# Performance work log

Measured on AMD Instinct MI355X. Metric: run time of the kernel, lower is better.

Reference implementation:

```python
import jax, jax.numpy as jnp
import numpy as np

DIM = 384
HEADS = 6
K = 3  # kernel_size, stride = 1


def setup_inputs() -> dict:
    key = jax.random.key(0)
    ks = jax.random.split(key, 7)
    B, H, W, C = 16, 56, 56, DIM
    sc = 1.0 / np.sqrt(C)
    return {
        "x_map": jax.random.normal(ks[0], (B, H, W, C), dtype=jnp.float32),
        # Linear weights stored [in, out] (torch stores [out, in]; math identical)
        "W_attn": jax.random.normal(ks[1], (C, HEADS * K * K), dtype=jnp.float32) * sc,
        "b_attn": jax.random.normal(ks[2], (HEADS * K * K,), dtype=jnp.float32) * 0.02,
        "W_v": jax.random.normal(ks[3], (C, C), dtype=jnp.float32) * sc,
        "b_v": jax.random.normal(ks[4], (C,), dtype=jnp.float32) * 0.02,
        "W_proj": jax.random.normal(ks[5], (C, C), dtype=jnp.float32) * sc,
        "b_proj": jax.random.normal(ks[6], (C,), dtype=jnp.float32) * 0.02,
    }


def reference(x_map, W_attn, b_attn, W_v, b_v, W_proj, b_proj):
    B, H, W, C = x_map.shape
    k, heads = K, HEADS
    hd = C // heads
    pad = k // 2

    # attention logits per output pixel: [B, H*W, heads, k*k], softmax over window
    a = x_map @ W_attn + b_attn                     # [B,H,W,heads*k*k]
    a = jax.nn.softmax(a.reshape(B, H * W, heads, k * k), axis=-1)

    v = x_map @ W_v + b_v                           # [B,H,W,C]
    vp = jnp.pad(v, ((0, 0), (pad, pad), (pad, pad), (0, 0)))
    # k*k shifted views == F.unfold with row-major (ki,kj) kernel order
    patches = jnp.stack(
        [vp[:, i:i + H, j:j + W, :] for i in range(k) for j in range(k)],
        axis=3,
    )                                               # [B,H,W,k*k,C]
    patches = patches.reshape(B, H * W, k * k, heads, hd)

    # softmax-weighted sum over the k*k window, per head
    y = jnp.einsum('bpKhd,bphK->bphd', patches, a)  # [B,H*W,heads,hd]
    y = y.reshape(B, H, W, C)
    return y @ W_proj + b_proj
```

## Files before the change

### kernel.cpp

```cpp
#include <hip/hip_runtime.h>
#include <math.h>

#define NPIX 50176
#define CDIM 384
#define HEADS 6
#define NLOGIT 54
#define HH 56
#define WW 56

typedef __attribute__((ext_vector_type(8))) __bf16 bf16x8;
typedef __attribute__((ext_vector_type(4))) float f32x4;

__device__ __forceinline__ void glds16(const void* g, void* l) {
  __builtin_amdgcn_global_load_lds(
      (const __attribute__((address_space(1))) unsigned int*)g,
      (__attribute__((address_space(3))) unsigned int*)l, 16, 0, 0);
}

__global__ __launch_bounds__(256) void prep_kernel(
    const float* __restrict__ W_v, const float* __restrict__ W_proj,
    const float* __restrict__ W_attn, const float* __restrict__ b_attn,
    __bf16* __restrict__ Wtv, __bf16* __restrict__ Wtp,
    __bf16* __restrict__ Wta, float* __restrict__ bpad) {
  const int idx = blockIdx.x * 256 + threadIdx.x;
  const int WSZ = CDIM * CDIM;
  if (idx < WSZ) {
    const int n = idx / CDIM, k = idx % CDIM;
    Wtv[idx] = (__bf16)W_v[k * CDIM + n];
    Wtp[idx] = (__bf16)W_proj[k * CDIM + n];
  } else if (idx < WSZ + 64 * CDIM) {
    const int r = idx - WSZ;
    const int n = r / CDIM, k = r % CDIM;
    Wta[r] = (__bf16)((n < NLOGIT) ? W_attn[k * NLOGIT + n] : 0.f);
  } else if (idx < WSZ + 64 * CDIM + 64) {
    const int n = idx - WSZ - 64 * CDIM;
    bpad[n] = (n < NLOGIT) ? b_attn[n] : 0.f;
  }
}

__global__ __launch_bounds__(256) void gemm_v_logit_kernel(
    const float* __restrict__ X, const __bf16* __restrict__ Wtv,
    const float* __restrict__ b_v, __bf16* __restrict__ v,
    const __bf16* __restrict__ Wta, const float* __restrict__ bpad,
    float* __restrict__ attn) {
  __shared__ char smem[34816];
  __bf16 (*As)[32] = (__bf16(*)[32])smem;
  __bf16 (*Bs)[32] = (__bf16(*)[32])(smem + 8192);
  float (*Ls)[68]  = (float(*)[68])smem;

  const int tid  = threadIdx.x;
  const int wave = tid >> 6;
  const int lane = tid & 63;
  const int bm   = blockIdx.x * 128;
  const int lrow  = lane >> 2;
  const int lkoff = (lane & 3) * 8;
  const int frow  = lane & 15;
  const int fk    = (lane >> 4) * 8;

  const bool is_logit = (blockIdx.y == 3);
  const int bn = is_logit ? 0 : blockIdx.y * 128;
  const int wr = (wave >> 1) * 64;
  const int wc = (wave & 1) * 64;

  f32x4 acc[4][4] = {};

  for (int k0 = 0; k0 < CDIM; k0 += 32) {
    const float* gx = X + (size_t)(bm + wave * 32 + lrow) * CDIM + k0 + lkoff;
    const float4 f0 = *(const float4*)(gx + 0);
    const float4 f1 = *(const float4*)(gx + 4);
    const float4 f2 = *(const float4*)(gx + 16 * CDIM + 0);
    const float4 f3 = *(const float4*)(gx + 16 * CDIM + 4);

    if (is_logit) {
      const __bf16* gb = Wta + (size_t)(wave * 16 + lrow) * CDIM + k0 + lkoff;
      glds16(gb, &Bs[wave * 16][0]);
    } else {
      const __bf16* gb = Wtv + (size_t)(bn + wave * 32 + lrow) * CDIM + k0 + lkoff;
      glds16(gb,                     &Bs[wave * 32][0]);
      glds16(gb + 16 * (size_t)CDIM, &Bs[wave * 32 + 16][0]);
    }

    bf16x8 h0, h1;
    h0[0] = (__bf16)f0.x; h0[1] = (__bf16)f0.y; h0[2] = (__bf16)f0.z; h0[3] = (__bf16)f0.w;
    h0[4] = (__bf16)f1.x; h0[5] = (__bf16)f1.y; h0[6] = (__bf16)f1.z; h0[7] = (__bf16)f1.w;
    h1[0] = (__bf16)f2.x; h1[1] = (__bf16)f2.y; h1[2] = (__bf16)f2.z; h1[3] = (__bf16)f2.w;
    h1[4] = (__bf16)f3.x; h1[5] = (__bf16)f3.y; h1[6] = (__bf16)f3.z; h1[7] = (__bf16)f3.w;
    *(bf16x8*)&As[wave * 32 + lrow][lkoff]      = h0;
    *(bf16x8*)&As[wave * 32 + 16 + lrow][lkoff] = h1;
    __syncthreads();

    if (is_logit) {
      bf16x8 a[2], b[4];
      #pragma unroll
      for (int mi = 0; mi < 2; ++mi)
        a[mi] = *(const bf16x8*)&As[wave * 32 + mi * 16 + frow][fk];
      #pragma unroll
      for (int ni = 0; ni < 4; ++ni)
        b[ni] = *(const bf16x8*)&Bs[ni * 16 + frow][fk];
      #pragma unroll
      for (int mi = 0; mi < 2; ++mi)
        #pragma unroll
        for (int ni = 0; ni < 4; ++ni)
          acc[mi][ni] = __builtin_amdgcn_mfma_f32_16x16x32_bf16(
              a[mi], b[ni], acc[mi][ni], 0, 0, 0);
    } else {
      bf16x8 a[4], b[4];
      #pragma unroll
      for (int mi = 0; mi < 4; ++mi)
        a[mi] = *(const bf16x8*)&As[wr + mi * 16 + frow][fk];
      #pragma unroll
      for (int ni = 0; ni < 4; ++ni)
        b[ni] = *(const bf16x8*)&Bs[wc + ni * 16 + frow][fk];
      #pragma unroll
      for (int mi = 0; mi < 4; ++mi)
        #pragma unroll
        for (int ni = 0; ni < 4; ++ni)
          acc[mi][ni] = __builtin_amdgcn_mfma_f32_16x16x32_bf16(
              a[mi], b[ni], acc[mi][ni], 0, 0, 0);
    }
    __syncthreads();
  }

  if (!is_logit) {
    const int orow = (lane >> 4) * 4;
    #pragma unroll
    for (int mi = 0; mi < 4; ++mi) {
      #pragma unroll
      for (int ni = 0; ni < 4; ++ni) {
        const int n = bn + wc + ni * 16 + frow;
        const float bvl = b_v[n];
        #pragma unroll
        for (int r = 0; r < 4; ++r) {
          const int m = bm + wr + mi * 16 + orow + r;
          v[(size_t)m * CDIM + n] = (__bf16)(acc[mi][ni][r] + bvl);
        }
      }
    }
  } else {
    float bvl[4];
    #pragma unroll
    for (int ni = 0; ni < 4; ++ni) bvl[ni] = bpad[ni * 16 + frow];
    const int orow = (lane >> 4) * 4;
    #pragma unroll
    for (int mi = 0; mi < 2; ++mi)
      #pragma unroll
      for (int ni = 0; ni < 4; ++ni)
        #pragma unroll
        for (int r = 0; r < 4; ++r)
          Ls[wave * 32 + mi * 16 + orow + r][ni * 16 + frow] =
              acc[mi][ni][r] + bvl[ni];
    __syncthreads();

    #pragma unroll
    for (int it = 0; it < 3; ++it) {
      const int task = it * 256 + tid;
      const int pl = task / HEADS;
      const int h  = task % HEADS;
      const float* row = &Ls[pl][h * 9];
      float m = row[0];
      #pragma unroll
      for (int w = 1; w < 9; ++w) m = fmaxf(m, row[w]);
      float e[9], s = 0.f;
      #pragma unroll
      for (int w = 0; w < 9; ++w) { e[w] = __expf(row[w] - m); s += e[w]; }
      const float inv = 1.f / s;
      float* op = &attn[(size_t)(bm + pl) * NLOGIT + h * 9];
      #pragma unroll
      for (int w = 0; w < 9; ++w) op[w] = e[w] * inv;
    }
  }
}

__global__ __launch_bounds__(256) void gemm_proj_kernel(
    const __bf16* __restrict__ A, const __bf16* __restrict__ Bt,
    const float* __restrict__ bias, float* __restrict__ Out) {
  __shared__ __bf16 As[128][32];
  __shared__ __bf16 Bs[128][32];

  const int tid  = threadIdx.x;
  const int wave = tid >> 6;
  const int lane = tid & 63;
  const int bm = blockIdx.x * 128;
  const int bn = blockIdx.y * 128;

  const int lrow  = lane >> 2;
  const int lkoff = (lane & 3) * 8;
  const int frow  = lane & 15;
  const int fk    = (lane >> 4) * 8;
  const int wr = (wave >> 1) * 64;
  const int wc = (wave & 1) * 64;

  f32x4 acc[4][4] = {};

  for (int k0 = 0; k0 < CDIM; k0 += 32) {
    const __bf16* ga = A  + (size_t)(bm + wave * 32 + lrow) * CDIM + k0 + lkoff;
    const __bf16* gb = Bt + (size_t)(bn + wave * 32 + lrow) * CDIM + k0 + lkoff;
    glds16(ga,                     &As[wave * 32][0]);
    glds16(ga + 16 * (size_t)CDIM, &As[wave * 32 + 16][0]);
    glds16(gb,                     &Bs[wave * 32][0]);
    glds16(gb + 16 * (size_t)CDIM, &Bs[wave * 32 + 16][0]);
    __syncthreads();

    bf16x8 a[4], b[4];
    #pragma unroll
    for (int mi = 0; mi < 4; ++mi)
      a[mi] = *(const bf16x8*)&As[wr + mi * 16 + frow][fk];
    #pragma unroll
    for (int ni = 0; ni < 4; ++ni)
      b[ni] = *(const bf16x8*)&Bs[wc + ni * 16 + frow][fk];
    #pragma unroll
    for (int mi = 0; mi < 4; ++mi)
      #pragma unroll
      for (int ni = 0; ni < 4; ++ni)
        acc[mi][ni] = __builtin_amdgcn_mfma_f32_16x16x32_bf16(
            a[mi], b[ni], acc[mi][ni], 0, 0, 0);
    __syncthreads();
  }

  const int orow = (lane >> 4) * 4;
  #pragma unroll
  for (int mi = 0; mi < 4; ++mi) {
    #pragma unroll
    for (int ni = 0; ni < 4; ++ni) {
      const int n = bn + wc + ni * 16 + frow;
      const float bvl = bias[n];
      #pragma unroll
      for (int r = 0; r < 4; ++r) {
        const int m = bm + wr + mi * 16 + orow + r;
        Out[(size_t)m * CDIM + n] = acc[mi][ni][r] + bvl;
      }
    }
  }
}

__global__ __launch_bounds__(256) void aggregate_kernel(
    const __bf16* __restrict__ v, const float* __restrict__ attn,
    __bf16* __restrict__ y) {
  const int idx = blockIdx.x * 256 + threadIdx.x;
  const int cg = idx % 48;
  const int pg = idx / 48;
  const int c  = cg * 8;
  const int b  = pg / ((HH / 4) * WW);
  const int r2 = pg % ((HH / 4) * WW);
  const int i0 = (r2 / WW) * 4;
  const int j  = r2 % WW;
  const int head = c >> 6;

  const int pbase = (b * HH + i0) * WW + j;
  float aw[4][9];
  #pragma unroll
  for (int p = 0; p < 4; ++p) {
    const float* ap = attn + (size_t)(pbase + p * WW) * NLOGIT + head * 9;
    #pragma unroll
    for (int w = 0; w < 9; ++w) aw[p][w] = ap[w];
  }

  const bool j0ok = (j > 0), j2ok = (j < WW - 1);
  float acc[4][8] = {};

  #pragma unroll
  for (int li = 0; li < 6; ++li) {
    const int ii = i0 - 1 + li;
    if (ii < 0 || ii >= HH) continue;
    const __bf16* vrow = v + ((size_t)(b * HH + ii) * WW + j) * CDIM + c;
    float ch[3][8];
    #pragma unroll
    for (int kj = 0; kj < 3; ++kj) {
      const bool ok = (kj == 0) ? j0ok : (kj == 2) ? j2ok : true;
      if (ok) {
        const bf16x8 vv = *(const bf16x8*)(vrow + (kj - 1) * CDIM);
        #pragma unroll
        for (int q = 0; q < 8; ++q) ch[kj][q] = (float)vv[q];
      } else {
        #pragma unroll
        for (int q = 0; q < 8; ++q) ch[kj][q] = 0.f;
      }
    }
    #pragma unroll
    for (int p = 0; p < 4; ++p) {
      const int ki = li - p;
      if (ki < 0 || ki > 2) continue;
      #pragma unroll
      for (int kj = 0; kj < 3; ++kj) {
        const float w = aw[p][ki * 3 + kj];
        #pragma unroll
        for (int q = 0; q < 8; ++q) acc[p][q] += w * ch[kj][q];
      }
    }
  }

  #pragma unroll
  for (int p = 0; p < 4; ++p) {
    bf16x8 o;
    #pragma unroll
    for (int q = 0; q < 8; ++q) o[q] = (__bf16)acc[p][q];
    *(bf16x8*)&y[(size_t)(pbase + p * WW) * CDIM + c] = o;
  }
}

extern "C" void kernel_launch(void* const* d_in, const int* in_sizes, int n_in,
                              void* d_out, int out_size, void* d_ws,
                              size_t ws_size, hipStream_t stream) {
  const float* x      = (const float*)d_in[0];
  const float* W_attn = (const float*)d_in[1];
  const float* b_attn = (const float*)d_in[2];
  const float* W_v    = (const float*)d_in[3];
  const float* b_v    = (const float*)d_in[4];
  const float* W_proj = (const float*)d_in[5];
  const float* b_proj = (const float*)d_in[6];
  float* out = (float*)d_out;

  char* w = (char*)d_ws;
  __bf16* v    = (__bf16*)w;  w += (size_t)NPIX * CDIM * 2;
  __bf16* y    = (__bf16*)w;  w += (size_t)NPIX * CDIM * 2;
  float*  attn = (float*)w;   w += (size_t)NPIX * NLOGIT * 4;
  __bf16* Wta  = (__bf16*)w;  w += 64 * CDIM * 2;
  float*  bpad = (float*)w;   w += 64 * 4;
  __bf16* Wtv  = (__bf16*)w;  w += CDIM * CDIM * 2;
  __bf16* Wtp  = (__bf16*)w;  w += CDIM * CDIM * 2;

  const int prep_n = CDIM * CDIM + 64 * CDIM + 64;
  prep_kernel<<<(prep_n + 255) / 256, 256, 0, stream>>>(
      W_v, W_proj, W_attn, b_attn, Wtv, Wtp, Wta, bpad);

  gemm_v_logit_kernel<<<dim3(NPIX / 128, 4), 256, 0, stream>>>(
      x, Wtv, b_v, v, Wta, bpad, attn);

  aggregate_kernel<<<(NPIX / 4 * 48) / 256, 256, 0, stream>>>(v, attn, y);

  gemm_proj_kernel<<<dim3(NPIX / 128, CDIM / 128), 256, 0, stream>>>(
      y, Wtp, b_proj, out);
}
```

Before: 126.6 us.

## Use full-width N tiles so X is read once per GEMM, concatenating V and logit weights

Concatenates the V and attention-logit weight matrices into one 448-row operand. Each block now computes 64 rows across the full output width (448 or 384 columns), so the fp32 input X is loaded and converted only once instead of four times. The projection GEMM is tiled the same way. The X loads for the next k-step are also prefetched into registers. In exchange each wave holds 28 or 24 accumulator tiles, which raises register pressure and can lower occupancy, and every block restreams the whole weight matrix through LDS.

```diff
diff --git a/kernel.cpp b/kernel.cpp
--- a/kernel.cpp
+++ b/kernel.cpp
@@ -7,6 +7,7 @@
 #define NLOGIT 54
 #define HH 56
 #define WW 56
+#define NCAT 448
 
 typedef __attribute__((ext_vector_type(8))) __bf16 bf16x8;
 typedef __attribute__((ext_vector_type(4))) float f32x4;
@@ -20,140 +21,107 @@
 __global__ __launch_bounds__(256) void prep_kernel(
     const float* __restrict__ W_v, const float* __restrict__ W_proj,
     const float* __restrict__ W_attn, const float* __restrict__ b_attn,
-    __bf16* __restrict__ Wtv, __bf16* __restrict__ Wtp,
-    __bf16* __restrict__ Wta, float* __restrict__ bpad) {
+    __bf16* __restrict__ Wcat, __bf16* __restrict__ Wtp,
+    float* __restrict__ bpad) {
   const int idx = blockIdx.x * 256 + threadIdx.x;
-  const int WSZ = CDIM * CDIM;
-  if (idx < WSZ) {
+  const int CATSZ = NCAT * CDIM;
+  const int WSZ   = CDIM * CDIM;
+  if (idx < CATSZ) {
     const int n = idx / CDIM, k = idx % CDIM;
-    Wtv[idx] = (__bf16)W_v[k * CDIM + n];
-    Wtp[idx] = (__bf16)W_proj[k * CDIM + n];
-  } else if (idx < WSZ + 64 * CDIM) {
-    const int r = idx - WSZ;
+    float val;
+    if (n < CDIM) val = W_v[k * CDIM + n];
+    else {
+      const int nn = n - CDIM;
+      val = (nn < NLOGIT) ? W_attn[k * NLOGIT + nn] : 0.f;
+    }
+    Wcat[idx] = (__bf16)val;
+  } else if (idx < CATSZ + WSZ) {
+    const int r = idx - CATSZ;
     const int n = r / CDIM, k = r % CDIM;
-    Wta[r] = (__bf16)((n < NLOGIT) ? W_attn[k * NLOGIT + n] : 0.f);
-  } else if (idx < WSZ + 64 * CDIM + 64) {
-    const int n = idx - WSZ - 64 * CDIM;
+    Wtp[r] = (__bf16)W_proj[k * CDIM + n];
+  } else if (idx < CATSZ + WSZ + 64) {
+    const int n = idx - CATSZ - WSZ;
     bpad[n] = (n < NLOGIT) ? b_attn[n] : 0.f;
   }
 }
 
 __global__ __launch_bounds__(256) void gemm_v_logit_kernel(
-    const float* __restrict__ X, const __bf16* __restrict__ Wtv,
+    const float* __restrict__ X, const __bf16* __restrict__ Wcat,
     const float* __restrict__ b_v, __bf16* __restrict__ v,
-    const __bf16* __restrict__ Wta, const float* __restrict__ bpad,
-    float* __restrict__ attn) {
-  __shared__ char smem[34816];
-  __bf16 (*As)[32] = (__bf16(*)[32])smem;
-  __bf16 (*Bs)[32] = (__bf16(*)[32])(smem + 8192);
+    const float* __restrict__ bpad, float* __restrict__ attn) {
+  __shared__ char smem[33792];
+  __bf16 (*As)[40] = (__bf16(*)[40])smem;
+  __bf16 (*Bs)[32] = (__bf16(*)[32])(smem + 5120);
   float (*Ls)[68]  = (float(*)[68])smem;
 
   const int tid  = threadIdx.x;
   const int wave = tid >> 6;
   const int lane = tid & 63;
-  const int bm   = blockIdx.x * 128;
-  const int lrow  = lane >> 2;
-  const int lkoff = (lane & 3) * 8;
+  const int bm   = blockIdx.x * 64;
+  const int srow  = lane >> 2;
+  const int skoff = (lane & 3) * 8;
   const int frow  = lane & 15;
   const int fk    = (lane >> 4) * 8;
-
-  const bool is_logit = (blockIdx.y == 3);
-  const int bn = is_logit ? 0 : blockIdx.y * 128;
-  const int wr = (wave >> 1) * 64;
-  const int wc = (wave & 1) * 64;
-
-  f32x4 acc[4][4] = {};
-
-  for (int k0 = 0; k0 < CDIM; k0 += 32) {
-    const float* gx = X + (size_t)(bm + wave * 32 + lrow) * CDIM + k0 + lkoff;
-    const float4 f0 = *(const float4*)(gx + 0);
-    const float4 f1 = *(const float4*)(gx + 4);
-    const float4 f2 = *(const float4*)(gx + 16 * CDIM + 0);
-    const float4 f3 = *(const float4*)(gx + 16 * CDIM + 4);
-
-    if (is_logit) {
-      const __bf16* gb = Wta + (size_t)(wave * 16 + lrow) * CDIM + k0 + lkoff;
-      glds16(gb, &Bs[wave * 16][0]);
-    } else {
-      const __bf16* gb = Wtv + (size_t)(bn + wave * 32 + lrow) * CDIM + k0 + lkoff;
-      glds16(gb,                     &Bs[wave * 32][0]);
-      glds16(gb + 16 * (size_t)CDIM, &Bs[wave * 32 + 16][0]);
-    }
-
-    bf16x8 h0, h1;
-    h0[0] = (__bf16)f0.x; h0[1] = (__bf16)f0.y; h0[2] = (__bf16)f0.z; h0[3] = (__bf16)f0.w;
-    h0[4] = (__bf16)f1.x; h0[5] = (__bf16)f1.y; h0[6] = (__bf16)f1.z; h0[7] = (__bf16)f1.w;
-    h1[0] = (__bf16)f2.x; h1[1] = (__bf16)f2.y; h1[2] = (__bf16)f2.z; h1[3] = (__bf16)f2.w;
-    h1[4] = (__bf16)f3.x; h1[5] = (__bf16)f3.y; h1[6] = (__bf16)f3.z; h1[7] = (__bf16)f3.w;
-    *(bf16x8*)&As[wave * 32 + lrow][lkoff]      = h0;
-    *(bf16x8*)&As[wave * 32 + 16 + lrow][lkoff] = h1;
-    __syncthreads();
-
-    if (is_logit) {
-      bf16x8 a[2], b[4];
-      #pragma unroll
-      for (int mi = 0; mi < 2; ++mi)
-        a[mi] = *(const bf16x8*)&As[wave * 32 + mi * 16 + frow][fk];
-      #pragma unroll
-      for (int ni = 0; ni < 4; ++ni)
-        b[ni] = *(const bf16x8*)&Bs[ni * 16 + frow][fk];
-      #pragma unroll
-      for (int mi = 0; mi < 2; ++mi)
-        #pragma unroll
-        for (int ni = 0; ni < 4; ++ni)
-          acc[mi][ni] = __builtin_amdgcn_mfma_f32_16x16x32_bf16(
-              a[mi], b[ni], acc[mi][ni], 0, 0, 0);
-    } else {
-      bf16x8 a[4], b[4];
-      #pragma unroll
-      for (int mi = 0; mi < 4; ++mi)
-        a[mi] = *(const bf16x8*)&As[wr + mi * 16 + frow][fk];
-      #pragma unroll
-      for (int ni = 0; ni < 4; ++ni)
-        b[ni] = *(const bf16x8*)&Bs[wc + ni * 16 + frow][fk];
-      #pragma unroll
-      for (int mi = 0; mi < 4; ++mi)
-        #pragma unroll
-        for (int ni = 0; ni < 4; ++ni)
-          acc[mi][ni] = __builtin_amdgcn_mfma_f32_16x16x32_bf16(
-              a[mi], b[ni], acc[mi][ni], 0, 0, 0);
-    }
-    __syncthreads();
-  }
-
-  if (!is_logit) {
-    const int orow = (lane >> 4) * 4;
-    #pragma unroll
-    for (int mi = 0; mi < 4; ++mi) {
-      #pragma unroll
-      for (int ni = 0; ni < 4; ++ni) {
-        const int n = bn + wc + ni * 16 + frow;
-        const float bvl = b_v[n];
-        #pragma unroll
-        for (int r = 0; r < 4; ++r) {
-          const int m = bm + wr + mi * 16 + orow + r;
-          v[(size_t)m * CDIM + n] = (__bf16)(acc[mi][ni][r] + bvl);
-        }
-      }
-    }
-  } else {
-    float bvl[4];
-    #pragma unroll
-    for (int ni = 0; ni < 4; ++ni) bvl[ni] = bpad[ni * 16 + frow];
-    const int orow = (lane >> 4) * 4;
-    #pragma unroll
-    for (int mi = 0; mi < 2; ++mi)
-      #pragma unroll
-      for (int ni = 0; ni < 4; ++ni)
-        #pragma unroll
-        for (int r = 0; r < 4; ++r)
-          Ls[wave * 32 + mi * 16 + orow + r][ni * 16 + frow] =
-              acc[mi][ni][r] + bvl[ni];
-    __syncthreads();
-
-    #pragma unroll
-    for (int it = 0; it < 3; ++it) {
-      const int task = it * 256 + tid;
+  const size_t xrow = (size_t)(bm + wave * 16 + srow) * CDIM;
+
+  f32x4 acc[28] = {};
+
+  float4 pa0 = *(const float4*)(X + xrow + skoff);
+  float4 pa1 = *(const float4*)(X + xrow + skoff + 4);
+
+  for (int ks = 0; ks < 12; ++ks) {
+    const int k0 = ks * 32;
+    #pragma unroll
+    for (int c = 0; c < 7; ++c) {
+      const int brow = wave * 112 + c * 16;
+      glds16(Wcat + (size_t)(brow + srow) * CDIM + k0 + skoff, &Bs[brow][0]);
+    }
+    bf16x8 h;
+    h[0] = (__bf16)pa0.x; h[1] = (__bf16)pa0.y; h[2] = (__bf16)pa0.z; h[3] = (__bf16)pa0.w;
+    h[4] = (__bf16)pa1.x; h[5] = (__bf16)pa1.y; h[6] = (__bf16)pa1.z; h[7] = (__bf16)pa1.w;
+    *(bf16x8*)&As[wave * 16 + srow][skoff] = h;
+    if (ks < 11) {
+      pa0 = *(const float4*)(X + xrow + k0 + 32 + skoff);
+      pa1 = *(const float4*)(X + xrow + k0 + 36 + skoff);
+    }
+    __syncthreads();
+
+    const bf16x8 a = *(const bf16x8*)&As[wave * 16 + frow][fk];
+    #pragma unroll
+    for (int ni = 0; ni < 28; ++ni) {
+      const bf16x8 b = *(const bf16x8*)&Bs[ni * 16 + frow][fk];
+      acc[ni] = __builtin_amdgcn_mfma_f32_16x16x32_bf16(a, b, acc[ni], 0, 0, 0);
+    }
+    __syncthreads();
+  }
+
+  const int orow = (lane >> 4) * 4;
+
+  #pragma unroll
+  for (int ni = 0; ni < 24; ++ni) {
+    const int n = ni * 16 + frow;
+    const float bvl = b_v[n];
+    #pragma unroll
+    for (int r = 0; r < 4; ++r) {
+      const int m = bm + wave * 16 + orow + r;
+      v[(size_t)m * CDIM + n] = (__bf16)(acc[ni][r] + bvl);
+    }
+  }
+
+  float bvl[4];
+  #pragma unroll
+  for (int ni = 0; ni < 4; ++ni) bvl[ni] = bpad[ni * 16 + frow];
+  #pragma unroll
+  for (int ni = 0; ni < 4; ++ni)
+    #pragma unroll
+    for (int r = 0; r < 4; ++r)
+      Ls[wave * 16 + orow + r][ni * 16 + frow] = acc[24 + ni][r] + bvl[ni];
+  __syncthreads();
+
+  #pragma unroll
+  for (int it = 0; it < 2; ++it) {
+    const int task = it * 256 + tid;
+    if (task < 64 * HEADS) {
       const int pl = task / HEADS;
       const int h  = task % HEADS;
       const float* row = &Ls[pl][h * 9];
@@ -174,61 +142,49 @@
 __global__ __launch_bounds__(256) void gemm_proj_kernel(
     const __bf16* __restrict__ A, const __bf16* __restrict__ Bt,
     const float* __restrict__ bias, float* __restrict__ Out) {
-  __shared__ __bf16 As[128][32];
-  __shared__ __bf16 Bs[128][32];
+  __shared__ __bf16 As[64][32];
+  __shared__ __bf16 Bs[384][32];
 
   const int tid  = threadIdx.x;
   const int wave = tid >> 6;
   const int lane = tid & 63;
-  const int bm = blockIdx.x * 128;
-  const int bn = blockIdx.y * 128;
-
-  const int lrow  = lane >> 2;
-  const int lkoff = (lane & 3) * 8;
+  const int bm   = blockIdx.x * 64;
+  const int srow  = lane >> 2;
+  const int skoff = (lane & 3) * 8;
   const int frow  = lane & 15;
   const int fk    = (lane >> 4) * 8;
-  const int wr = (wave >> 1) * 64;
-  const int wc = (wave & 1) * 64;
-
-  f32x4 acc[4][4] = {};
-
-  for (int k0 = 0; k0 < CDIM; k0 += 32) {
-    const __bf16* ga = A  + (size_t)(bm + wave * 32 + lrow) * CDIM + k0 + lkoff;
-    const __bf16* gb = Bt + (size_t)(bn + wave * 32 + lrow) * CDIM + k0 + lkoff;
-    glds16(ga,                     &As[wave * 32][0]);
-    glds16(ga + 16 * (size_t)CDIM, &As[wave * 32 + 16][0]);
-    glds16(gb,                     &Bs[wave * 32][0]);
-    glds16(gb + 16 * (size_t)CDIM, &Bs[wave * 32 + 16][0]);
-    __syncthreads();
-
-    bf16x8 a[4], b[4];
-    #pragma unroll
-    for (int mi = 0; mi < 4; ++mi)
-      a[mi] = *(const bf16x8*)&As[wr + mi * 16 + frow][fk];
-    #pragma unroll
-    for (int ni = 0; ni < 4; ++ni)
-      b[ni] = *(const bf16x8*)&Bs[wc + ni * 16 + frow][fk];
-    #pragma unroll
-    for (int mi = 0; mi < 4; ++mi)
-      #pragma unroll
-      for (int ni = 0; ni < 4; ++ni)
-        acc[mi][ni] = __builtin_amdgcn_mfma_f32_16x16x32_bf16(
-            a[mi], b[ni], acc[mi][ni], 0, 0, 0);
+
+  f32x4 acc[24] = {};
+
+  for (int ks = 0; ks < 12; ++ks) {
+    const int k0 = ks * 32;
+    glds16(A + (size_t)(bm + wave * 16 + srow) * CDIM + k0 + skoff,
+           &As[wave * 16][0]);
+    #pragma unroll
+    for (int c = 0; c < 6; ++c) {
+      const int brow = wave * 96 + c * 16;
+      glds16(Bt + (size_t)(brow + srow) * CDIM + k0 + skoff, &Bs[brow][0]);
+    }
+    __syncthreads();
+
+    const bf16x8 a = *(const bf16x8*)&As[wave * 16 + frow][fk];
+    #pragma unroll
+    for (int ni = 0; ni < 24; ++ni) {
+      const bf16x8 b = *(const bf16x8*)&Bs[ni * 16 + frow][fk];
+      acc[ni] = __builtin_amdgcn_mfma_f32_16x16x32_bf16(a, b, acc[ni], 0, 0, 0);
+    }
     __syncthreads();
   }
 
   const int orow = (lane >> 4) * 4;
   #pragma unroll
-  for (int mi = 0; mi < 4; ++mi) {
-    #pragma unroll
-    for (int ni = 0; ni < 4; ++ni) {
-      const int n = bn + wc + ni * 16 + frow;
-      const float bvl = bias[n];
-      #pragma unroll
-      for (int r = 0; r < 4; ++r) {
-        const int m = bm + wr + mi * 16 + orow + r;
-        Out[(size_t)m * CDIM + n] = acc[mi][ni][r] + bvl;
-      }
+  for (int ni = 0; ni < 24; ++ni) {
+    const int n = ni * 16 + frow;
+    const float bvl = bias[n];
+    #pragma unroll
+    for (int r = 0; r < 4; ++r) {
+      const int m = bm + wave * 16 + orow + r;
+      Out[(size_t)m * CDIM + n] = acc[ni][r] + bvl;
     }
   }
 }
@@ -314,20 +270,18 @@
   __bf16* v    = (__bf16*)w;  w += (size_t)NPIX * CDIM * 2;
   __bf16* y    = (__bf16*)w;  w += (size_t)NPIX * CDIM * 2;
   float*  attn = (float*)w;   w += (size_t)NPIX * NLOGIT * 4;
-  __bf16* Wta  = (__bf16*)w;  w += 64 * CDIM * 2;
+  __bf16* Wcat = (__bf16*)w;  w += (size_t)NCAT * CDIM * 2;
+  __bf16* Wtp  = (__bf16*)w;  w += (size_t)CDIM * CDIM * 2;
   float*  bpad = (float*)w;   w += 64 * 4;
-  __bf16* Wtv  = (__bf16*)w;  w += CDIM * CDIM * 2;
-  __bf16* Wtp  = (__bf16*)w;  w += CDIM * CDIM * 2;
-
-  const int prep_n = CDIM * CDIM + 64 * CDIM + 64;
+
+  const int prep_n = NCAT * CDIM + CDIM * CDIM + 64;
   prep_kernel<<<(prep_n + 255) / 256, 256, 0, stream>>>(
-      W_v, W_proj, W_attn, b_attn, Wtv, Wtp, Wta, bpad);
-
-  gemm_v_logit_kernel<<<dim3(NPIX / 128, 4), 256, 0, stream>>>(
-      x, Wtv, b_v, v, Wta, bpad, attn);
+      W_v, W_proj, W_attn, b_attn, Wcat, Wtp, bpad);
+
+  gemm_v_logit_kernel<<<NPIX / 64, 256, 0, stream>>>(
+      x, Wcat, b_v, v, bpad, attn);
 
   aggregate_kernel<<<(NPIX / 4 * 48) / 256, 256, 0, stream>>>(v, attn, y);
 
-  gemm_proj_kernel<<<dim3(NPIX / 128, CDIM / 128), 256, 0, stream>>>(
-      y, Wtp, b_proj, out);
-}
+  gemm_proj_kernel<<<NPIX / 64, 256, 0, stream>>>(y, Wtp, b_proj, out);
+}
```

Result: faster. 119.4 us (-5.7%).
